# Optimization experiments

Measured on AMD Instinct MI355X. Metric: run time of the kernel, lower is better.

The kernel has to match this reference:

```python
import jax, jax.numpy as jnp
import numpy as np

BS, N, FIN = 128, 320, 1
H1, F1 = 8, 18   # layer-1 heads / hidden
H2, F2 = 4, 46   # layer-2 heads / hidden
D1 = H1 * F1     # 144
D2 = H2 * F2     # 184
FC = (104, 45, 84)
ALPHA = 0.2
NEG = -9e15


def _xavier(key, shape):
    fan_in, fan_out = shape[-2], shape[-1]
    s = 1.414 * np.sqrt(2.0 / (fan_in + fan_out))
    return jax.random.normal(key, shape, dtype=jnp.float32) * s


def setup_inputs() -> dict:
    key = jax.random.key(0)
    ks = jax.random.split(key, 20)
    xnodes = jax.random.normal(ks[0], (BS, N, FIN), dtype=jnp.float32)
    adj = (jax.random.uniform(ks[1], (N, N)) < 0.1).astype(jnp.float32)
    adj = jnp.maximum(adj, jnp.eye(N, dtype=jnp.float32))
    inp = {
        'xnodes': xnodes,
        'adj': adj,
        'W1': _xavier(ks[2], (H1, FIN, F1)),
        'a1': _xavier(ks[3], (H1, 2 * F1)),
        'W2': _xavier(ks[4], (H2, D1, F2)),
        'a2': _xavier(ks[5], (H2, 2 * F2)),
        'p1w': _xavier(ks[6], (D1, 1))[:, 0],
        'p1b': jnp.zeros((), jnp.float32),
        'p2w': _xavier(ks[7], (D2, 1))[:, 0],
        'p2b': jnp.zeros((), jnp.float32),
        'e1w': _xavier(ks[8], (3 * N, FC[0])),
        'e1b': jnp.zeros((FC[0],), jnp.float32),
        'e2w': _xavier(ks[9], (FC[0], FC[1])),
        'e2b': jnp.zeros((FC[1],), jnp.float32),
        'e3w': _xavier(ks[10], (FC[1], FC[2])),
        'e3b': jnp.zeros((FC[2],), jnp.float32),
        'cw': _xavier(ks[11], (FC[2], 1))[:, 0],
        'cb': jnp.zeros((), jnp.float32),
    }
    return inp


def _gat(x, adj_mask, W, a):
    """Multi-head GAT layer (all heads vectorized).
    x: [b,n,fin], W: [h,fin,f], a: [h,2f], adj_mask: [n,n] bool.
    Score e_ij = leakyrelu(a_src.h_i + a_dst.h_j) == concat-matmul of the
    original, without materializing the [b,n,n,2f] tensor.
    """
    h = jnp.einsum('bni,hif->bhnf', x, W)              # [b,h,n,f]
    f = h.shape[-1]
    es = jnp.einsum('bhnf,hf->bhn', h, a[:, :f])       # source term
    ed = jnp.einsum('bhnf,hf->bhn', h, a[:, f:])       # dest term
    e = jax.nn.leaky_relu(es[:, :, :, None] + ed[:, :, None, :], ALPHA)
    e = jnp.where(adj_mask[None, None], e, NEG)
    att = jax.nn.softmax(e, axis=-1)                   # [b,h,n,n]
    hp = jnp.einsum('bhnm,bhmf->bhnf', att, h)
    out = jax.nn.elu(hp)                               # concat=True
    b = out.shape[0]
    return out.transpose(0, 2, 1, 3).reshape(b, out.shape[2], -1)  # [b,n,h*f]


def reference(xnodes, adj, W1, a1, W2, a2, p1w, p1b, p2w, p2b,
              e1w, e1b, e2w, e2b, e3w, e3b, cw, cb):
    mask = adj > 0
    x0 = jnp.mean(xnodes, axis=-1)                     # [b,n]
    x = _gat(xnodes, mask, W1, a1)                     # [b,n,144]
    x1 = x @ p1w + p1b                                 # pool1 -> [b,n]
    x = _gat(x, mask, W2, a2)                          # [b,n,184]
    x2 = x @ p2w + p2b                                 # pool2 -> [b,n]
    x_concat = jnp.concatenate([x0, x1, x2], axis=1)   # [b,3n]
    h = jax.nn.elu(x_concat @ e1w + e1b)
    h = jax.nn.elu(h @ e2w + e2b)
    features = jax.nn.elu(h @ e3w + e3b)               # [b,84]
    hazard = (features @ cw + cb).reshape(-1)          # [b]
    return (x_concat, features, hazard)
```

## Files before the change

### kernel.cpp

```cpp
#include <hip/hip_runtime.h>
#include <hip/hip_bf16.h>
#include <math.h>

#define BS 128
#define NN 320
#define H1 8
#define F1 18
#define H2C 4
#define F2 46
#define FC0 104
#define FC1 45
#define FC2 84
#define LRA 0.2f
#define DEGCAP 96
#define PW 104

typedef __attribute__((ext_vector_type(8))) short bf16x8;
typedef __attribute__((ext_vector_type(4))) float f32x4;

__device__ __forceinline__ float wave_max64(float v) {
    #pragma unroll
    for (int off = 32; off > 0; off >>= 1)
        v = fmaxf(v, __shfl_xor(v, off, 64));
    return v;
}
__device__ __forceinline__ short bfb(float x) {
    __hip_bfloat16 b = __float2bfloat16(x);
    return *(short*)&b;
}

__global__ void k_csr(const float* __restrict__ adj,
                      unsigned short* __restrict__ cols16,
                      unsigned short* __restrict__ colsT16,
                      int4* __restrict__ meta, const float* __restrict__ W1,
                      const float* __restrict__ a1, float* __restrict__ c1s,
                      float* __restrict__ c1d, const float* __restrict__ W2,
                      __hip_bfloat16* __restrict__ Bb) {
    int row = blockIdx.x;
    int lane = threadIdx.x;
    if (row < NN) {
        int base = 0, c96 = 0, c192 = 0, c288 = 0;
        for (int c0 = 0; c0 < NN; c0 += 64) {
            int j = c0 + lane;
            bool p = (j < NN) && (adj[row * NN + j] > 0.f);
            unsigned long long m = __ballot(p);
            if (p) {
                int pos = base + __popcll(m & ((1ull << lane) - 1ull));
                if (pos < DEGCAP) {
                    cols16[row * DEGCAP + pos] = (unsigned short)j;
                    colsT16[pos * NN + row] = (unsigned short)j;
                }
            }
            base += __popcll(m);
            c96  += __popcll(__ballot(p && j < 96));
            c192 += __popcll(__ballot(p && j < 192));
            c288 += __popcll(__ballot(p && j < 288));
        }
        if (base > DEGCAP) base = DEGCAP;
        if (c96 > DEGCAP) c96 = DEGCAP;
        if (c192 > DEGCAP) c192 = DEGCAP;
        if (c288 > DEGCAP) c288 = DEGCAP;
        for (int q = base + lane; q < DEGCAP; q += 64) {
            cols16[row * DEGCAP + q] = 0;
            colsT16[q * NN + row] = 0;
        }
        if (lane == 0) meta[row] = make_int4(c96, c192, c288, base);
    } else if (row == NN) {
        int h = lane;
        if (h < H1) {
            float s = 0.f, d = 0.f;
            for (int f = 0; f < F1; ++f) {
                float w = W1[h * F1 + f];
                s += w * a1[h * 2 * F1 + f];
                d += w * a1[h * 2 * F1 + F1 + f];
            }
            c1s[h] = s;
            c1d[h] = d;
        }
    } else {
        int idx = (row - NN - 1) * 64 + lane;
        int e = idx & 7;
        int t = idx >> 3;
        int n = t % 192, k8 = t / 192;
        int k = k8 * 8 + e, hh = n / 48, f = n - hh * 48;
        float v = (k < 144 && f < 46) ? W2[(hh * 144 + k) * 46 + f] : 0.f;
        Bb[idx] = __float2bfloat16(v);
    }
}

__global__ __launch_bounds__(320) void k_l1(
    const float* __restrict__ xn, const unsigned short* __restrict__ colsT16,
    const int4* __restrict__ meta, const float* __restrict__ W1,
    const float* __restrict__ c1s, const float* __restrict__ c1d,
    const float* __restrict__ p1w, __hip_bfloat16* __restrict__ out1b,
    float* __restrict__ part1) {
    int bx = blockIdx.x;
    int k = bx & 7, slot = bx >> 3;
    int b = k + 8 * (slot >> 3);
    int h = slot & 7;
    __shared__ float xb[NN];
    __shared__ float w1h[F1], pwl[F1];
    __shared__ float redmax[5], redmin[5];
    int tid = threadIdx.x;
    int wv = tid >> 6, lane = tid & 63;
    float xi = xn[b * NN + tid];
    xb[tid] = xi;
    if (tid < F1) { w1h[tid] = W1[h * F1 + tid]; pwl[tid] = p1w[h * F1 + tid]; }
    int Li = meta[tid].w;
    float mx = wave_max64(xi);
    float mn = -wave_max64(-xi);
    int Lmax = (int)wave_max64((float)Li);
    if (lane == 0) { redmax[wv] = mx; redmin[wv] = mn; }
    __syncthreads();
    float MX = redmax[0], MN = redmin[0];
    #pragma unroll
    for (int q = 1; q < 5; ++q) {
        MX = fmaxf(MX, redmax[q]);
        MN = fminf(MN, redmin[q]);
    }
    float cs = c1s[h], cd = c1d[h];
    float u = xi * cs;
    float mt = u + (cd > 0.f ? cd * MX : cd * MN);
    float m = fmaxf(mt, LRA * mt);
    float num = 0.f, den = 0.f;
    const unsigned short* ct = colsT16 + tid;
    int colv = ct[0];
    for (int j = 0; j < Lmax; ++j) {
        int coln = (j + 1 < Lmax) ? ct[(j + 1) * NN] : 0;
        float xj = xb[colv];
        bool act = j < Li;
        float t = fmaf(xj, cd, u);
        t = fmaxf(t, LRA * t);
        float w = __expf(t - m);
        w = act ? w : 0.f;
        num = fmaf(w, xj, num);
        den += w;
        colv = coln;
    }
    float s = num / den;
    float part = 0.f;
    unsigned od[9];
    #pragma unroll
    for (int f = 0; f < F1; f += 2) {
        float v0 = s * w1h[f];
        v0 = v0 > 0.f ? v0 : __expf(v0) - 1.f;
        float v1 = s * w1h[f + 1];
        v1 = v1 > 0.f ? v1 : __expf(v1) - 1.f;
        part = fmaf(v0, pwl[f], part);
        part = fmaf(v1, pwl[f + 1], part);
        od[f >> 1] = (unsigned)(unsigned short)bfb(v0) |
                     ((unsigned)(unsigned short)bfb(v1) << 16);
    }
    __hip_bfloat16* rowp = out1b + (size_t)(b * NN + tid) * 160;
    unsigned* dst = (unsigned*)(rowp + h * F1);
    #pragma unroll
    for (int q = 0; q < 9; ++q) dst[q] = od[q];
    if (h == 0) {
        uint4 z = (uint4){0u, 0u, 0u, 0u};
        *(uint4*)(rowp + 144) = z;
        *(uint4*)(rowp + 152) = z;
    }
    part1[(size_t)(b * 8 + h) * NN + tid] = part;
}

__global__ __launch_bounds__(256) void k_l2(
    const __hip_bfloat16* __restrict__ out1b,
    const unsigned short* __restrict__ cols16,
    const int4* __restrict__ meta, const __hip_bfloat16* __restrict__ Bb,
    const float* __restrict__ a2, const float* __restrict__ p2w,
    float* __restrict__ part2) {
    int bx = blockIdx.x;
    int k = bx & 7, slot = bx >> 3;
    int b = k + 8 * (slot >> 3);
    int h = (slot >> 1) & 3;
    int rh = slot & 1;
    int bh = b * 4 + h;
    __shared__ __align__(16) __hip_bfloat16 HT[48][328];
    __shared__ __align__(16) __hip_bfloat16 AsP[4][16][PW];
    __shared__ float esl[NN], edl[NN];
    __shared__ float denW[4][16];
    __shared__ float pwl[48], a2e[48], a2d[48];
    __shared__ float Mred[4];
    int tid = threadIdx.x, wv = tid >> 6, lane = tid & 63;
    int lr = lane & 15, lq = lane >> 4;
    if (tid < 48) {
        pwl[tid] = tid < 46 ? p2w[h * F2 + tid] : 0.f;
        a2e[tid] = tid < 46 ? a2[h * 92 + tid] : 0.f;
        a2d[tid] = tid < 46 ? a2[h * 92 + 46 + tid] : 0.f;
    }
    bf16x8 bq[5][3];
    #pragma unroll
    for (int kc = 0; kc < 5; ++kc)
        #pragma unroll
        for (int t = 0; t < 3; ++t)
            bq[kc][t] = *(const bf16x8*)(Bb +
                (size_t)(((kc * 4 + lq) * 192) + h * 48 + t * 16 + lr) * 8);
    __syncthreads();
    const __hip_bfloat16* Ag = out1b + (size_t)b * NN * 160;
    for (int tile = 0; tile < 5; ++tile) {
        int r0 = tile * 64;
        const __hip_bfloat16* arow = Ag + (size_t)(r0 + wv * 16 + lr) * 160 + lq * 8;
        f32x4 acc[3];
        #pragma unroll
        for (int t = 0; t < 3; ++t) acc[t] = (f32x4){0.f, 0.f, 0.f, 0.f};
        #pragma unroll
        for (int kc = 0; kc < 5; ++kc) {
            bf16x8 a = *(const bf16x8*)(arow + kc * 32);
            #pragma unroll
            for (int t = 0; t < 3; ++t)
                acc[t] = __builtin_amdgcn_mfma_f32_16x16x32_bf16(
                    a, bq[kc][t], acc[t], 0, 0, 0);
        }
        int node = r0 + wv * 16 + lq * 4;
        #pragma unroll
        for (int t = 0; t < 3; ++t) {
            short4 s4;
            s4.x = bfb(acc[t][0]); s4.y = bfb(acc[t][1]);
            s4.z = bfb(acc[t][2]); s4.w = bfb(acc[t][3]);
            *(short4*)&HT[t * 16 + lr][node] = s4;
        }
        float esa[4] = {0.f, 0.f, 0.f, 0.f}, eda[4] = {0.f, 0.f, 0.f, 0.f};
        #pragma unroll
        for (int t = 0; t < 3; ++t) {
            float ae = a2e[t * 16 + lr], ad = a2d[t * 16 + lr];
            #pragma unroll
            for (int j = 0; j < 4; ++j) {
                esa[j] = fmaf(acc[t][j], ae, esa[j]);
                eda[j] = fmaf(acc[t][j], ad, eda[j]);
            }
        }
        #pragma unroll
        for (int j = 0; j < 4; ++j) {
            #pragma unroll
            for (int off = 1; off < 16; off <<= 1) {
                esa[j] += __shfl_xor(esa[j], off, 64);
                eda[j] += __shfl_xor(eda[j], off, 64);
            }
        }
        if (lr == 0) {
            #pragma unroll
            for (int j = 0; j < 4; ++j) {
                esl[node + j] = esa[j];
                edl[node + j] = eda[j];
            }
        }
    }
    __syncthreads();
    float edmax = -1e30f;
    for (int i = tid; i < NN; i += 256) edmax = fmaxf(edmax, edl[i]);
    float wm = wave_max64(edmax);
    if (lane == 0) Mred[wv] = wm;
    __syncthreads();
    float M = fmaxf(fmaxf(Mred[0], Mred[1]), fmaxf(Mred[2], Mred[3]));
    int t0i = rh ? 2 : 0;
    int t1i = rh ? 5 : 2;
    for (int tile = t0i; tile < t1i; ++tile) {
        int r0 = tile * 64;
        int i = r0 + wv * 16 + lr;
        int4 mt = meta[i];
        int sb0 = mt.x, sb1 = mt.y, sb2 = mt.z, sb3 = mt.w;
        float es = esl[i];
        float t0 = es + M;
        float m = fmaxf(t0, LRA * t0);
        const unsigned short* crow = cols16 + (size_t)i * DEGCAP;
        f32x4 acc[3];
        #pragma unroll
        for (int t = 0; t < 3; ++t) acc[t] = (f32x4){0.f, 0.f, 0.f, 0.f};
        float dp = 0.f;
        #pragma unroll
        for (int pass = 0; pass < 4; ++pass) {
            for (int q = lane; q < 192; q += 64) {
                int rr = q / 12, cc = q - rr * 12;
                *(uint4*)&AsP[wv][rr][cc * 8] = (uint4){0u, 0u, 0u, 0u};
            }
            int s0 = pass == 0 ? 0 : (pass == 1 ? sb0 : (pass == 2 ? sb1 : sb2));
            int s1 = pass == 0 ? sb0 : (pass == 1 ? sb1 : (pass == 2 ? sb2 : sb3));
            int pofs = pass * 96;
            int j = s0 + lq;
            int col = (j < s1) ? crow[j] : 0;
            for (; j < s1; j += 4) {
                int coln = (j + 4 < s1) ? crow[j + 4] : 0;
                float t = es + edl[col];
                t = fmaxf(t, LRA * t);
                float w = __expf(t - m);
                dp += w;
                AsP[wv][lr][col - pofs] = __float2bfloat16(w);
                col = coln;
            }
            const int nkf = (pass < 3) ? 3 : 1;
            #pragma unroll
            for (int kf = 0; kf < nkf; ++kf) {
                bf16x8 a = *(const bf16x8*)&AsP[wv][lr][kf * 32 + lq * 8];
                #pragma unroll
                for (int t = 0; t < 3; ++t) {
                    bf16x8 bb = *(const bf16x8*)&HT[t * 16 + lr][pofs + kf * 32 + lq * 8];
                    acc[t] = __builtin_amdgcn_mfma_f32_16x16x32_bf16(
                        a, bb, acc[t], 0, 0, 0);
                }
            }
        }
        dp += __shfl_xor(dp, 16, 64);
        dp += __shfl_xor(dp, 32, 64);
        if (lq == 0) denW[wv][lr] = dp;
        float inv[4], part[4];
        #pragma unroll
        for (int j = 0; j < 4; ++j) {
            inv[j] = 1.f / denW[wv][lq * 4 + j];
            part[j] = 0.f;
        }
        #pragma unroll
        for (int t = 0; t < 3; ++t) {
            float pw = pwl[t * 16 + lr];
            #pragma unroll
            for (int j = 0; j < 4; ++j) {
                float v = acc[t][j] * inv[j];
                v = v > 0.f ? v : __expf(v) - 1.f;
                part[j] = fmaf(v, pw, part[j]);
            }
        }
        #pragma unroll
        for (int j = 0; j < 4; ++j) {
            #pragma unroll
            for (int off = 1; off < 16; off <<= 1)
                part[j] += __shfl_xor(part[j], off, 64);
        }
        if (lr == 0) {
            #pragma unroll
            for (int j = 0; j < 4; ++j)
                part2[(size_t)bh * NN + r0 + wv * 16 + lq * 4 + j] = part[j];
        }
    }
}

__global__ __launch_bounds__(256) void k_head(
    const float* __restrict__ xn, const float* __restrict__ part1,
    const float* __restrict__ part2, const float* __restrict__ p1b,
    const float* __restrict__ p2b, const float* __restrict__ e1w,
    const float* __restrict__ e1b, const float* __restrict__ e2w,
    const float* __restrict__ e2b, const float* __restrict__ e3w,
    const float* __restrict__ e3b, const float* __restrict__ cw,
    const float* __restrict__ cb, float* __restrict__ dout) {
    int b = blockIdx.x;
    int tid = threadIdx.x;
    __shared__ float xc[960];
    __shared__ float e1part[2][FC0];
    __shared__ float h1[FC0];
    __shared__ float hh[FC1];
    __shared__ float ft[FC2];
    for (int t = tid; t < NN; t += 256) {
        float x0 = xn[b * NN + t];
        xc[t] = x0;
        dout[b * 960 + t] = x0;
        float s1 = p1b[0];
        #pragma unroll
        for (int h = 0; h < 8; ++h) s1 += part1[(size_t)(b * 8 + h) * NN + t];
        xc[320 + t] = s1;
        dout[b * 960 + 320 + t] = s1;
        float s2 = p2b[0];
        #pragma unroll
        for (int h = 0; h < 4; ++h) s2 += part2[(size_t)(b * 4 + h) * NN + t];
        xc[640 + t] = s2;
        dout[b * 960 + 640 + t] = s2;
    }
    __syncthreads();
    {
        int half = tid >> 7, o = tid & 127;
        if (o < FC0) {
            float a = 0.f;
            int k0 = half * 480;
            for (int k = k0; k < k0 + 480; ++k)
                a = fmaf(xc[k], e1w[k * FC0 + o], a);
            e1part[half][o] = a;
        }
    }
    __syncthreads();
    if (tid < FC0) {
        float a = e1b[tid] + e1part[0][tid] + e1part[1][tid];
        h1[tid] = a > 0.f ? a : expm1f(a);
    }
    __syncthreads();
    if (tid < FC1) {
        float a = e2b[tid];
        for (int k = 0; k < FC0; ++k) a += h1[k] * e2w[k * FC1 + tid];
        hh[tid] = a > 0.f ? a : expm1f(a);
    }
    __syncthreads();
    if (tid < FC2) {
        float a = e3b[tid];
        for (int k = 0; k < FC1; ++k) a += hh[k] * e3w[k * FC2 + tid];
        a = a > 0.f ? a : expm1f(a);
        ft[tid] = a;
        dout[BS * 960 + b * FC2 + tid] = a;
    }
    __syncthreads();
    if (tid < 64) {
        float v = 0.f;
        for (int t = tid; t < FC2; t += 64) v += ft[t] * cw[t];
        #pragma unroll
        for (int off = 32; off > 0; off >>= 1) v += __shfl_xor(v, off, 64);
        if (tid == 0) dout[BS * 960 + BS * FC2 + b] = v + cb[0];
    }
}

extern "C" void kernel_launch(void* const* d_in, const int* in_sizes, int n_in,
                              void* d_out, int out_size, void* d_ws,
                              size_t ws_size, hipStream_t stream) {
    const float* xn  = (const float*)d_in[0];
    const float* adj = (const float*)d_in[1];
    const float* W1  = (const float*)d_in[2];
    const float* a1  = (const float*)d_in[3];
    const float* W2  = (const float*)d_in[4];
    const float* a2  = (const float*)d_in[5];
    const float* p1w = (const float*)d_in[6];
    const float* p1b = (const float*)d_in[7];
    const float* p2w = (const float*)d_in[8];
    const float* p2b = (const float*)d_in[9];
    const float* e1w = (const float*)d_in[10];
    const float* e1b = (const float*)d_in[11];
    const float* e2w = (const float*)d_in[12];
    const float* e2b = (const float*)d_in[13];
    const float* e3w = (const float*)d_in[14];
    const float* e3b = (const float*)d_in[15];
    const float* cw  = (const float*)d_in[16];
    const float* cb  = (const float*)d_in[17];

    char* ws = (char*)d_ws;
    int4*  meta     = (int4*)ws;
    float* c1s      = (float*)(ws + 5120);
    float* c1d      = (float*)(ws + 5152);
    unsigned short* cols16  = (unsigned short*)(ws + 5248);
    unsigned short* colsT16 = (unsigned short*)(ws + 66688);
    __hip_bfloat16* Bb = (__hip_bfloat16*)(ws + 128128);
    __hip_bfloat16* out1b = (__hip_bfloat16*)(ws + 189568);
    float* part1    = (float*)(ws + 13296768);
    float* part2    = (float*)(ws + 14607488);
    float* dout     = (float*)d_out;

    k_csr<<<NN + 1 + 480, 64, 0, stream>>>(adj, cols16, colsT16, meta,
                                           W1, a1, c1s, c1d, W2, Bb);
    k_l1<<<BS * H1, 320, 0, stream>>>(xn, colsT16, meta, W1, c1s, c1d,
                                      p1w, out1b, part1);
    k_l2<<<BS * H2C * 2, 256, 0, stream>>>(out1b, cols16, meta, Bb, a2, p2w, part2);
    k_head<<<BS, 256, 0, stream>>>(xn, part1, part2, p1b, p2b, e1w, e1b,
                                   e2w, e2b, e3w, e3b, cw, cb, dout);
}
```

Before: 178.4 us.

## Process all row tiles per GAT layer-2 block and use two wider column passes

The layer-2 kernel no longer splits each (batch, head) across two blocks. One block now covers all five 64-row tiles, which halves the grid and avoids recomputing the shared H projection and score prologue twice. The sparse attention column loop now runs in two 192-wide passes instead of four 96-wide ones, using the 192-column boundary and the degree from the meta array. This cuts zeroing and sync rounds, but the larger LDS tile may lower occupancy, and halving the block count reduces parallelism across compute units.

```diff
diff --git a/kernel.cpp b/kernel.cpp
--- a/kernel.cpp
+++ b/kernel.cpp
@@ -13,7 +13,8 @@
 #define FC2 84
 #define LRA 0.2f
 #define DEGCAP 96
-#define PW 104
+#define HW 328
+#define APW 200
 
 typedef __attribute__((ext_vector_type(8))) short bf16x8;
 typedef __attribute__((ext_vector_type(4))) float f32x4;
@@ -171,12 +172,11 @@
     float* __restrict__ part2) {
     int bx = blockIdx.x;
     int k = bx & 7, slot = bx >> 3;
-    int b = k + 8 * (slot >> 3);
-    int h = (slot >> 1) & 3;
-    int rh = slot & 1;
+    int b = k + 8 * (slot >> 2);
+    int h = slot & 3;
     int bh = b * 4 + h;
-    __shared__ __align__(16) __hip_bfloat16 HT[48][328];
-    __shared__ __align__(16) __hip_bfloat16 AsP[4][16][PW];
+    __shared__ __align__(16) __hip_bfloat16 HT[48][HW];
+    __shared__ __align__(16) __hip_bfloat16 AsP[4][16][APW];
     __shared__ float esl[NN], edl[NN];
     __shared__ float denW[4][16];
     __shared__ float pwl[48], a2e[48], a2d[48];
@@ -252,13 +252,11 @@
     if (lane == 0) Mred[wv] = wm;
     __syncthreads();
     float M = fmaxf(fmaxf(Mred[0], Mred[1]), fmaxf(Mred[2], Mred[3]));
-    int t0i = rh ? 2 : 0;
-    int t1i = rh ? 5 : 2;
-    for (int tile = t0i; tile < t1i; ++tile) {
+    for (int tile = 0; tile < 5; ++tile) {
         int r0 = tile * 64;
         int i = r0 + wv * 16 + lr;
         int4 mt = meta[i];
-        int sb0 = mt.x, sb1 = mt.y, sb2 = mt.z, sb3 = mt.w;
+        int c192 = mt.y, deg = mt.w;
         float es = esl[i];
         float t0 = es + M;
         float m = fmaxf(t0, LRA * t0);
@@ -268,14 +266,14 @@
         for (int t = 0; t < 3; ++t) acc[t] = (f32x4){0.f, 0.f, 0.f, 0.f};
         float dp = 0.f;
         #pragma unroll
-        for (int pass = 0; pass < 4; ++pass) {
-            for (int q = lane; q < 192; q += 64) {
-                int rr = q / 12, cc = q - rr * 12;
+        for (int pass = 0; pass < 2; ++pass) {
+            for (int q = lane; q < 400; q += 64) {
+                int rr = q / 25, cc = q - rr * 25;
                 *(uint4*)&AsP[wv][rr][cc * 8] = (uint4){0u, 0u, 0u, 0u};
             }
-            int s0 = pass == 0 ? 0 : (pass == 1 ? sb0 : (pass == 2 ? sb1 : sb2));
-            int s1 = pass == 0 ? sb0 : (pass == 1 ? sb1 : (pass == 2 ? sb2 : sb3));
-            int pofs = pass * 96;
+            int s0 = pass ? c192 : 0;
+            int s1 = pass ? deg : c192;
+            int pofs = pass * 192;
             int j = s0 + lq;
             int col = (j < s1) ? crow[j] : 0;
             for (; j < s1; j += 4) {
@@ -287,9 +285,10 @@
                 AsP[wv][lr][col - pofs] = __float2bfloat16(w);
                 col = coln;
             }
-            const int nkf = (pass < 3) ? 3 : 1;
-            #pragma unroll
-            for (int kf = 0; kf < nkf; ++kf) {
+            const int nkf = pass ? 4 : 6;
+            #pragma unroll
+            for (int kf = 0; kf < 6; ++kf) {
+                if (kf >= nkf) break;
                 bf16x8 a = *(const bf16x8*)&AsP[wv][lr][kf * 32 + lq * 8];
                 #pragma unroll
                 for (int t = 0; t < 3; ++t) {
@@ -304,30 +303,30 @@
         if (lq == 0) denW[wv][lr] = dp;
         float inv[4], part[4];
         #pragma unroll
-        for (int j = 0; j < 4; ++j) {
-            inv[j] = 1.f / denW[wv][lq * 4 + j];
-            part[j] = 0.f;
+        for (int j2 = 0; j2 < 4; ++j2) {
+            inv[j2] = 1.f / denW[wv][lq * 4 + j2];
+            part[j2] = 0.f;
         }
         #pragma unroll
         for (int t = 0; t < 3; ++t) {
             float pw = pwl[t * 16 + lr];
             #pragma unroll
-            for (int j = 0; j < 4; ++j) {
-                float v = acc[t][j] * inv[j];
+            for (int j2 = 0; j2 < 4; ++j2) {
+                float v = acc[t][j2] * inv[j2];
                 v = v > 0.f ? v : __expf(v) - 1.f;
-                part[j] = fmaf(v, pw, part[j]);
-            }
-        }
-        #pragma unroll
-        for (int j = 0; j < 4; ++j) {
+                part[j2] = fmaf(v, pw, part[j2]);
+            }
+        }
+        #pragma unroll
+        for (int j2 = 0; j2 < 4; ++j2) {
             #pragma unroll
             for (int off = 1; off < 16; off <<= 1)
-                part[j] += __shfl_xor(part[j], off, 64);
+                part[j2] += __shfl_xor(part[j2], off, 64);
         }
         if (lr == 0) {
             #pragma unroll
-            for (int j = 0; j < 4; ++j)
-                part2[(size_t)bh * NN + r0 + wv * 16 + lq * 4 + j] = part[j];
+            for (int j2 = 0; j2 < 4; ++j2)
+                part2[(size_t)bh * NN + r0 + wv * 16 + lq * 4 + j2] = part[j2];
         }
     }
 }
@@ -440,7 +439,7 @@
                                            W1, a1, c1s, c1d, W2, Bb);
     k_l1<<<BS * H1, 320, 0, stream>>>(xn, colsT16, meta, W1, c1s, c1d,
                                       p1w, out1b, part1);
-    k_l2<<<BS * H2C * 2, 256, 0, stream>>>(out1b, cols16, meta, Bb, a2, p2w, part2);
+    k_l2<<<BS * H2C, 256, 0, stream>>>(out1b, cols16, meta, Bb, a2, p2w, part2);
     k_head<<<BS, 256, 0, stream>>>(xn, part1, part2, p1b, p2b, e1w, e1b,
                                    e2w, e2b, e3w, e3b, cw, cb, dout);
 }
```

New measurement: 168.5 us. -5.6%, faster.
